# Optimization experiments

Hardware: AMD Instinct MI355X
Metric: run time of the kernel (lower is better)

Reference implementation:

```python
import jax, jax.numpy as jnp
import numpy as np

MIN_NORM = 1e-15
BALL_EPS = 4e-3  # float32 boundary eps used by the PoincareBall manifold


def _norm(x):
    return jnp.maximum(jnp.linalg.norm(x, axis=-1, keepdims=True), MIN_NORM)


def _artanh(x):
    # clamp like torch Artanh autograd fn (1e-7 margin)
    return jnp.arctanh(jnp.clip(x, -1.0 + 1e-7, 1.0 - 1e-7))


def proj(x, c):
    n = _norm(x)
    maxnorm = (1.0 - BALL_EPS) / jnp.sqrt(c)
    return jnp.where(n > maxnorm, x / n * maxnorm, x)


def expmap0(u, c):
    sc = jnp.sqrt(c)
    n = _norm(u)
    return jnp.tanh(sc * n) * u / (sc * n)


def logmap0(p, c):
    sc = jnp.sqrt(c)
    n = _norm(p)
    return _artanh(sc * n) * p / (sc * n)


def mobius_add(x, y, c):
    x2 = jnp.sum(x * x, axis=-1, keepdims=True)
    y2 = jnp.sum(y * y, axis=-1, keepdims=True)
    xy = jnp.sum(x * y, axis=-1, keepdims=True)
    num = (1.0 + 2.0 * c * xy + c * y2) * x + (1.0 - c * x2) * y
    denom = 1.0 + 2.0 * c * xy + c * c * x2 * y2
    return num / jnp.maximum(denom, MIN_NORM)


def mobius_matvec(m, x, c):
    sc = jnp.sqrt(c)
    xn = _norm(x)
    mx = x @ m.T  # [N, out]
    mxn = _norm(mx)
    res = jnp.tanh(mxn / xn * _artanh(sc * xn)) * mx / (mxn * sc)
    is_zero = jnp.all(mx == 0, axis=-1, keepdims=True)
    return jnp.where(is_zero, jnp.zeros_like(res), res)


def setup_inputs() -> dict:
    key = jax.random.key(0)
    N, D_IN, D_OUT, E = 100000, 128, 128, 1600000
    k1, k2, k3, k4, k5 = jax.random.split(key, 5)
    # points inside the Poincare ball (||x|| ~ 0.34 < 1)
    x = 0.03 * jax.random.normal(k1, (N, D_IN), dtype=jnp.float32)
    # xavier_uniform with gain sqrt(2)
    limit = np.sqrt(2.0) * np.sqrt(6.0 / (D_IN + D_OUT))
    weight = jax.random.uniform(k2, (D_OUT, D_IN), minval=-limit, maxval=limit, dtype=jnp.float32)
    bias = jnp.zeros((D_OUT,), dtype=jnp.float32)
    edge_index = jax.random.randint(k3, (2, E), 0, N, dtype=jnp.int64)
    edge_weight = jax.random.uniform(k4, (E,), dtype=jnp.float32) / 16.0
    return {"x": x, "weight": weight, "bias": bias,
            "edge_index": edge_index, "edge_weight": edge_weight,
            "num_nodes": N}


def reference(x, weight, bias, edge_index, edge_weight, num_nodes):
    c_in = 1.0
    c_out = 1.0
    # --- OriginHypLinear (dropout=0 / eval) ---
    mv = proj(mobius_matvec(weight, x, c_in), c_in)
    hyp_bias = proj(expmap0(bias[None, :], c_in), c_in)  # proj_tan0 is identity
    h = proj(mobius_add(mv, hyp_bias, c_in), c_in)
    # --- OriginHypAgg: logmap0 -> spmm -> expmap0 ---
    xt = logmap0(h, c_in)
    dst, src = edge_index[0], edge_index[1]
    support = jax.ops.segment_sum(edge_weight[:, None] * xt[src], dst,
                                  num_segments=num_nodes)
    h = proj(expmap0(support, c_in), c_in)
    # --- OriginHypAct: relu in tangent space ---
    xt = jax.nn.relu(logmap0(h, c_in))  # proj_tan0 identity
    return proj(expmap0(xt, c_out), c_out)
```

## Files before the change

kernel.cpp:

```cpp
#include <hip/hip_runtime.h>
#include <math.h>

#define D 128
#define MAXNORM 0.996f
#define MINNORM 1e-15f
#define ATCLAMP (1.0f - 1e-7f)

#define CHUNK 2048
#define BSH   7
#define MAXNB 1024
#define SCAP  6144

typedef unsigned int   u32;
typedef unsigned short u16;

typedef __attribute__((ext_vector_type(8))) short bf16x8;
typedef __attribute__((ext_vector_type(4))) float f32x4;

__device__ __forceinline__ float wsum(float v) {
#pragma unroll
  for (int m = 32; m; m >>= 1) v += __shfl_xor(v, m);
  return v;
}
__device__ __forceinline__ float rsum16(float v) {
#pragma unroll
  for (int m = 1; m <= 8; m <<= 1) v += __shfl_xor(v, m);
  return v;
}

__device__ __forceinline__ float frcp(float x) { return __builtin_amdgcn_rcpf(x); }

__device__ __forceinline__ float fast_artanh(float x) {
  x = fminf(x, ATCLAMP);
  return 0.5f * __logf((1.0f + x) * frcp(1.0f - x));
}
__device__ __forceinline__ float fast_tanh(float z) {
  float t = __expf(-2.0f * z);
  return (1.0f - t) * frcp(1.0f + t);
}

__device__ __forceinline__ float bflo(u32 u) { return __uint_as_float(u << 16); }
__device__ __forceinline__ float bfhi(u32 u) { return __uint_as_float(u & 0xffff0000u); }
__device__ __forceinline__ u16 f2bf(float f) {
  u32 u = __float_as_uint(f);
  return (u16)((u + 0x7fffu + ((u >> 16) & 1u)) >> 16);
}
__device__ __forceinline__ float bf2f(u16 h) { return __uint_as_float(((u32)h) << 16); }

union U4B8 { uint4 u; bf16x8 b; };
__device__ __forceinline__ bf16x8 as_b8(uint4 v) { U4B8 c; c.u = v; return c.b; }

__device__ __forceinline__ bool detect_bf16(const u32* p) {
  float lo = fabsf(bflo(p[threadIdx.x & 63]));
  return (bool)__all(lo < 1.0f);
}
__device__ __forceinline__ bool detect_i64(const int* p) {
  return (bool)__all(p[2 * (threadIdx.x & 63) + 1] == 0);
}

template<bool BF>
__device__ __forceinline__ void k1_body(const void* xv, const void* Wv,
                                        const void* bv, u16* xt, int N,
                                        uint4* Wh, uint4* Wl) {
  const int tid  = threadIdx.x;
  const int lane = tid & 63;
  const int wid  = tid >> 6;
  const int qg   = lane >> 4;
  const int lc   = lane & 15;

  for (int slot = tid; slot < 2048; slot += 256) {
    const int l = slot & 63, frag = slot >> 6;
    const int t = frag >> 2, ks = frag & 3;
    const int j  = (l & 15) + 16 * t;
    const int k0 = 32 * ks + 8 * (l >> 4);
    if (BF) {
      Wh[slot] = ((const uint4*)Wv)[j * 16 + (k0 >> 3)];
    } else {
      const float* Wf = (const float*)Wv;
      float4 f0 = *(const float4*)(Wf + (size_t)j * D + k0);
      float4 f1 = *(const float4*)(Wf + (size_t)j * D + k0 + 4);
      float f[8] = {f0.x, f0.y, f0.z, f0.w, f1.x, f1.y, f1.z, f1.w};
      u32 hw[4], lw[4];
#pragma unroll
      for (int i = 0; i < 4; ++i) {
        u16 h0 = f2bf(f[2*i]),  h1 = f2bf(f[2*i+1]);
        u16 l0 = f2bf(f[2*i]   - bf2f(h0));
        u16 l1 = f2bf(f[2*i+1] - bf2f(h1));
        hw[i] = (u32)h0 | ((u32)h1 << 16);
        lw[i] = (u32)l0 | ((u32)l1 << 16);
      }
      Wh[slot] = make_uint4(hw[0], hw[1], hw[2], hw[3]);
      Wl[slot] = make_uint4(lw[0], lw[1], lw[2], lw[3]);
    }
  }

  float bfr[8];
  float nb2 = 0.f;
#pragma unroll
  for (int t = 0; t < 8; ++t) {
    float v = BF ? bf2f(((const u16*)bv)[lc + 16 * t])
                 : ((const float*)bv)[lc + 16 * t];
    bfr[t] = v; nb2 += v * v;
  }
  nb2 = rsum16(nb2);
  float y2;
  {
    float nb = fmaxf(sqrtf(nb2), MINNORM);
    float s  = fast_tanh(nb) * frcp(nb);
    float n1 = s * nb;
    if (n1 > MAXNORM) s *= MAXNORM * frcp(n1);
#pragma unroll
    for (int t = 0; t < 8; ++t) bfr[t] *= s;
    y2 = s * s * nb2;
  }
  const bool bias_zero = (y2 == 0.0f);

  __syncthreads();

  const int tile  = blockIdx.x * 4 + wid;
  const int rbase = tile * 16;
  if (rbase >= N) return;

  int rowA = rbase + lc; if (rowA >= N) rowA = N - 1;
  uint4 Ah[4], Al[4];
  float xn2 = 0.f;
  if (BF) {
    const uint4* xr = (const uint4*)((const u16*)xv + (size_t)rowA * D);
#pragma unroll
    for (int ks = 0; ks < 4; ++ks) {
      uint4 v = xr[4 * ks + qg];
      Ah[ks] = v;
      float a0 = bflo(v.x), a1 = bfhi(v.x), a2 = bflo(v.y), a3 = bfhi(v.y);
      float a4 = bflo(v.z), a5 = bfhi(v.z), a6 = bflo(v.w), a7 = bfhi(v.w);
      xn2 += a0*a0 + a1*a1 + a2*a2 + a3*a3 + a4*a4 + a5*a5 + a6*a6 + a7*a7;
    }
  } else {
    const float4* xr = (const float4*)((const float*)xv + (size_t)rowA * D);
#pragma unroll
    for (int ks = 0; ks < 4; ++ks) {
      float4 f0 = xr[8 * ks + 2 * qg], f1 = xr[8 * ks + 2 * qg + 1];
      float f[8] = {f0.x, f0.y, f0.z, f0.w, f1.x, f1.y, f1.z, f1.w};
      u32 hw[4], lw[4];
#pragma unroll
      for (int i = 0; i < 4; ++i) {
        u16 h0 = f2bf(f[2*i]),  h1 = f2bf(f[2*i+1]);
        u16 l0 = f2bf(f[2*i]   - bf2f(h0));
        u16 l1 = f2bf(f[2*i+1] - bf2f(h1));
        hw[i] = (u32)h0 | ((u32)h1 << 16);
        lw[i] = (u32)l0 | ((u32)l1 << 16);
        xn2 += f[2*i] * f[2*i] + f[2*i+1] * f[2*i+1];
      }
      Ah[ks] = make_uint4(hw[0], hw[1], hw[2], hw[3]);
      Al[ks] = make_uint4(lw[0], lw[1], lw[2], lw[3]);
    }
  }
  xn2 += __shfl_xor(xn2, 16);
  xn2 += __shfl_xor(xn2, 32);

  f32x4 acc[8];
  const f32x4 zero = {0.f, 0.f, 0.f, 0.f};
#pragma unroll
  for (int t = 0; t < 8; ++t) acc[t] = zero;
#pragma unroll
  for (int ks = 0; ks < 4; ++ks) {
    bf16x8 a = as_b8(Ah[ks]);
    bf16x8 al;
    if (!BF) al = as_b8(Al[ks]);
#pragma unroll
    for (int t = 0; t < 8; ++t) {
      const int idx = (t * 4 + ks) * 64 + lane;
      bf16x8 bh = as_b8(Wh[idx]);
      acc[t] = __builtin_amdgcn_mfma_f32_16x16x32_bf16(a, bh, acc[t], 0, 0, 0);
      if (!BF) {
        bf16x8 bl = as_b8(Wl[idx]);
        acc[t] = __builtin_amdgcn_mfma_f32_16x16x32_bf16(al, bh, acc[t], 0, 0, 0);
        acc[t] = __builtin_amdgcn_mfma_f32_16x16x32_bf16(a,  bl, acc[t], 0, 0, 0);
      }
    }
  }

#pragma unroll
  for (int q = 0; q < 4; ++q) {
    const int row_off = qg * 4 + q;
    const int row = rbase + row_off;
    float xnq = fmaxf(sqrtf(__shfl(xn2, row_off)), MINNORM);
    float s2 = 0.f;
#pragma unroll
    for (int t = 0; t < 8; ++t) { float v = acc[t][q]; s2 += v * v; }
    s2 = rsum16(s2);
    float mxn = fmaxf(sqrtf(s2), MINNORM);
    float r = fast_tanh(mxn * frcp(xnq) * fast_artanh(xnq)) * frcp(mxn);
    float pn = r * mxn;
    if (pn > MAXNORM) { r *= MAXNORM * frcp(pn); pn = MAXNORM; }
    float h[8];
    float hn;
    if (bias_zero) {
#pragma unroll
      for (int t = 0; t < 8; ++t) h[t] = r * acc[t][q];
      hn = pn;
    } else {
      float xy = 0.f;
#pragma unroll
      for (int t = 0; t < 8; ++t) { h[t] = r * acc[t][q]; xy += h[t] * bfr[t]; }
      xy = rsum16(xy);
      float x2 = pn * pn;
      float ca = 1.f + 2.f * xy + y2;
      float cb = 1.f - x2;
      float id = frcp(fmaxf(1.f + 2.f * xy + x2 * y2, MINNORM));
      float s3 = 0.f;
#pragma unroll
      for (int t = 0; t < 8; ++t) { h[t] = (ca * h[t] + cb * bfr[t]) * id; s3 += h[t] * h[t]; }
      hn = fmaxf(sqrtf(rsum16(s3)), MINNORM);
    }
    float ps = (hn > MAXNORM) ? (MAXNORM * frcp(hn)) : 1.f;
    float np = fmaxf(hn * ps, MINNORM);
    float tsc = fast_artanh(np) * frcp(np) * ps;
    if (row < N) {
      u16* xo = xt + (size_t)row * D + lc;
#pragma unroll
      for (int t = 0; t < 8; ++t) xo[16 * t] = f2bf(tsc * h[t]);
    }
  }
}

extern "C" __global__ __launch_bounds__(256)
void OriginHyperbolicGraphConvolution_38628935860614_kernel(
    const void* x, const void* W, const void* b, u16* xt, int N) {
  __shared__ uint4 Wh[2048];
  __shared__ uint4 Wl[2048];
  if (detect_bf16((const u32*)x)) k1_body<true >(x, W, b, xt, N, Wh, Wl);
  else                            k1_body<false>(x, W, b, xt, N, Wh, Wl);
}

extern "C" __global__ __launch_bounds__(256) void ksA(
    const int* ei, const void* ew, uint2* ebuck, u16* soffs, int E, int N, int nb) {
  __shared__ int   hist[MAXNB];
  __shared__ int   sArr[MAXNB + 1];
  __shared__ int   psum[256];
  __shared__ uint2 recs[CHUNK];
  const bool i64 = detect_i64(ei);
  const bool bf  = detect_bf16((const u32*)ew);
  const int tid   = threadIdx.x;
  const int cbase = blockIdx.x * CHUNK;

  for (int i = tid; i < MAXNB; i += 256) hist[i] = 0;
  __syncthreads();

  int bkt[8], rank[8]; u32 px[8], wb[8]; bool val[8];
#pragma unroll
  for (int r = 0; r < 8; ++r) {
    const int e = cbase + r * 256 + tid;
    val[r] = false;
    if (e < E) {
      int dst, src;
      if (i64) { dst = ei[2 * (size_t)e]; src = ei[2 * ((size_t)E + e)]; }
      else     { dst = ei[e];             src = ei[(size_t)E + e]; }
      if ((unsigned)dst < (unsigned)N && (unsigned)src < (unsigned)N) {
        val[r] = true;
        bkt[r] = dst >> BSH;
        px[r]  = (u32)src | ((u32)(dst & ((1 << BSH) - 1)) << 17);
        float w;
        if (bf) w = bf2f(((const u16*)ew)[e]); else w = ((const float*)ew)[e];
        wb[r] = __float_as_uint(w);
        rank[r] = atomicAdd(&hist[bkt[r]], 1);
      }
    }
  }
  __syncthreads();

  const int g0 = tid * 4;
  int loc[4], ts = 0;
#pragma unroll
  for (int i = 0; i < 4; ++i) { loc[i] = ts; ts += hist[g0 + i]; }
  psum[tid] = ts; __syncthreads();
#pragma unroll
  for (int off = 1; off < 256; off <<= 1) {
    int t = (tid >= off) ? psum[tid - off] : 0;
    __syncthreads();
    psum[tid] += t;
    __syncthreads();
  }
  const int excl = psum[tid] - ts;
#pragma unroll
  for (int i = 0; i < 4; ++i) sArr[g0 + i] = excl + loc[i];
  if (tid == 255) sArr[MAXNB] = psum[255];
  __syncthreads();

#pragma unroll
  for (int r = 0; r < 8; ++r) if (val[r])
    recs[sArr[bkt[r]] + rank[r]] = make_uint2(px[r], wb[r]);
  __syncthreads();

  const int vcnt = sArr[MAXNB];
  for (int i = tid; i < vcnt; i += 256) ebuck[(size_t)cbase + i] = recs[i];
  u16* so = soffs + (size_t)blockIdx.x * (nb + 1);
  for (int b = tid; b <= nb; b += 256) so[b] = (u16)sArr[b];
}

extern "C" __global__ __launch_bounds__(256) void ks2sum(
    const u16* soffs, int* btot, int nb, int nchunks) {
  __shared__ int red[256];
  const int b = blockIdx.x, tid = threadIdx.x;
  int s = 0;
  for (int c = tid; c < nchunks; c += 256) {
    const u16* so = soffs + (size_t)c * (nb + 1) + b;
    s += (int)so[1] - (int)so[0];
  }
  red[tid] = s; __syncthreads();
#pragma unroll
  for (int off = 128; off; off >>= 1) {
    if (tid < off) red[tid] += red[tid + off];
    __syncthreads();
  }
  if (tid == 0) btot[b] = red[0];
}

extern "C" __global__ __launch_bounds__(1024) void ks2scan(
    const int* btot, int* bbase, int nb) {
  __shared__ int sc[1024];
  const int t = threadIdx.x;
  int v = (t < nb) ? btot[t] : 0;
  sc[t] = v; __syncthreads();
#pragma unroll
  for (int off = 1; off < 1024; off <<= 1) {
    int u = (t >= off) ? sc[t - off] : 0;
    __syncthreads();
    sc[t] += u;
    __syncthreads();
  }
  if (t < nb) bbase[t] = sc[t] - v;
  if (t == 1023) bbase[nb] = sc[1023];
}

extern "C" __global__ __launch_bounds__(256) void ks3(
    const uint2* ebuck, const u16* soffs, const int* bbase,
    uint2* esrt, int* offs, int N, int nb, int nchunks) {
  __shared__ uint2 stage[SCAP];
  __shared__ int hist[128], sc[128], cur[128];
  __shared__ int lcur;
  const int tid = threadIdx.x;
  const int b = blockIdx.x;
  const int s0 = bbase[b], s1 = bbase[b + 1], sz = s1 - s0;
  if (tid < 128) hist[tid] = 0;
  if (tid == 0) lcur = 0;
  __syncthreads();

  const bool fit = (sz <= SCAP);
  if (fit) {
    for (int c = tid; c < nchunks; c += 256) {
      const u16* so = soffs + (size_t)c * (nb + 1) + b;
      const int a = so[0], e = so[1];
      if (e > a) {
        const int base = atomicAdd(&lcur, e - a);
        for (int j = a; j < e; ++j) {
          const uint2 r = ebuck[(size_t)c * CHUNK + j];
          stage[base + (j - a)] = r;
          atomicAdd(&hist[(r.x >> 17) & 127], 1);
        }
      }
    }
  } else {
    for (int c = tid; c < nchunks; c += 256) {
      const u16* so = soffs + (size_t)c * (nb + 1) + b;
      for (int j = so[0]; j < so[1]; ++j)
        atomicAdd(&hist[(ebuck[(size_t)c * CHUNK + j].x >> 17) & 127], 1);
    }
  }
  __syncthreads();

  int v = 0;
  if (tid < 128) { v = hist[tid]; sc[tid] = v; }
  __syncthreads();
#pragma unroll
  for (int off = 1; off < 128; off <<= 1) {
    int t = (tid < 128 && tid >= off) ? sc[tid - off] : 0;
    __syncthreads();
    if (tid < 128) sc[tid] += t;
    __syncthreads();
  }
  if (tid < 128) {
    const int st = sc[tid] - v;
    cur[tid] = st;
    const int node = (b << BSH) + tid;
    if (node < N) offs[node] = s0 + st;
  }
  if (tid == 0 && b == nb - 1) offs[N] = s1;
  __syncthreads();

  if (fit) {
    for (int i = tid; i < sz; i += 256) {
      const uint2 r = stage[i];
      const int d = atomicAdd(&cur[(r.x >> 17) & 127], 1);
      esrt[s0 + d] = make_uint2(r.x & 0x1FFFFu, r.y);
    }
  } else {
    for (int c = tid; c < nchunks; c += 256) {
      const u16* so = soffs + (size_t)c * (nb + 1) + b;
      for (int j = so[0]; j < so[1]; ++j) {
        const uint2 r = ebuck[(size_t)c * CHUNK + j];
        const int d = atomicAdd(&cur[(r.x >> 17) & 127], 1);
        esrt[s0 + d] = make_uint2(r.x & 0x1FFFFu, r.y);
      }
    }
  }
}

extern "C" __global__ __launch_bounds__(256) void kagg(
    const int* offs, const uint2* esrt, const u16* xt,
    void* out, const void* xdet, int N) {
  const bool bf = detect_bf16((const u32*)xdet);
  const int lane = threadIdx.x & 63;
  const int node = blockIdx.x * 4 + (threadIdx.x >> 6);
  if (node >= N) return;
  int s0 = __builtin_amdgcn_readfirstlane(offs[node]);
  int s1 = __builtin_amdgcn_readfirstlane(offs[node + 1]);
  const uint2* ep = esrt + s0;
  const int cnt = s1 - s0;
  const u32* xtw = (const u32*)xt;
  float a0 = 0.f, a1 = 0.f;
  int i = 0;
  for (; i + 8 <= cnt; i += 8) {
    uint2 e[8]; u32 u[8];
#pragma unroll
    for (int k = 0; k < 8; ++k) e[k] = ep[i + k];
#pragma unroll
    for (int k = 0; k < 8; ++k) u[k] = xtw[(e[k].x << 6) | lane];
#pragma unroll
    for (int k = 0; k < 8; ++k) {
      const float w = __uint_as_float(e[k].y);
      a0 += w * bflo(u[k]);
      a1 += w * bfhi(u[k]);
    }
  }
  for (; i + 4 <= cnt; i += 4) {
    uint2 e[4]; u32 u[4];
#pragma unroll
    for (int k = 0; k < 4; ++k) e[k] = ep[i + k];
#pragma unroll
    for (int k = 0; k < 4; ++k) u[k] = xtw[(e[k].x << 6) | lane];
#pragma unroll
    for (int k = 0; k < 4; ++k) {
      const float w = __uint_as_float(e[k].y);
      a0 += w * bflo(u[k]);
      a1 += w * bfhi(u[k]);
    }
  }
  for (; i < cnt; ++i) {
    const uint2 e = ep[i];
    const u32 u = xtw[(e.x << 6) | lane];
    const float w = __uint_as_float(e.y);
    a0 += w * bflo(u);
    a1 += w * bfhi(u);
  }
  float n = fmaxf(sqrtf(wsum(a0 * a0 + a1 * a1)), MINNORM);
  float tn = fast_tanh(n);
  float m = tn * frcp(n);
  if (tn > MAXNORM) { m *= MAXNORM * frcp(tn); tn = MAXNORM; }
  float nn = fmaxf(tn, MINNORM);
  m *= fast_artanh(nn) * frcp(nn);
  float tA = fmaxf(m * a0, 0.f), tB = fmaxf(m * a1, 0.f);
  float nr = fmaxf(sqrtf(wsum(tA * tA + tB * tB)), MINNORM);
  float t2 = fast_tanh(nr);
  float m2 = t2 * frcp(nr);
  if (t2 > MAXNORM) m2 *= MAXNORM * frcp(t2);
  float oA = m2 * tA, oB = m2 * tB;
  if (bf) {
    u32 o = ((u32)f2bf(oA)) | (((u32)f2bf(oB)) << 16);
    ((u32*)out)[(size_t)node * 64 + lane] = o;
  } else {
    ((float2*)out)[(size_t)node * 64 + lane] = make_float2(oA, oB);
  }
}

extern "C" void kernel_launch(void* const* d_in, const int* in_sizes, int n_in,
                              void* d_out, int out_size, void* d_ws, size_t ws_size,
                              hipStream_t stream) {
  const void* x    = d_in[0];
  const void* W    = d_in[1];
  const void* bias = d_in[2];
  const int*  ei   = (const int*)d_in[3];
  const void* ew   = d_in[4];
  const int N = in_sizes[0] / D;
  const int E = in_sizes[4];
  const int nchunks = (E + CHUNK - 1) / CHUNK;
  const int nb      = (N + (1 << BSH) - 1) >> BSH;

  char* ws = (char*)d_ws;
  size_t off = 0;
  auto carve = [&](size_t bytes) { char* p = ws + off; off = (off + bytes + 255) & ~(size_t)255; return p; };
  u16*   xt     = (u16*)  carve((size_t)N * D * sizeof(u16));
  uint2* ebuck  = (uint2*)carve((size_t)nchunks * CHUNK * sizeof(uint2));
  uint2* esrt   = (uint2*)carve((size_t)E * sizeof(uint2));
  u16*   soffs  = (u16*)  carve((size_t)nchunks * (nb + 1) * sizeof(u16));
  int*   btot   = (int*)  carve((size_t)nb * sizeof(int));
  int*   bbase  = (int*)  carve((size_t)(nb + 1) * sizeof(int));
  int*   offs   = (int*)  carve((size_t)(N + 1) * sizeof(int));

  OriginHyperbolicGraphConvolution_38628935860614_kernel<<<(N + 63) / 64, 256, 0, stream>>>(
      x, W, bias, xt, N);
  ksA   <<<nchunks, 256, 0, stream>>>(ei, ew, ebuck, soffs, E, N, nb);
  ks2sum<<<nb, 256, 0, stream>>>(soffs, btot, nb, nchunks);
  ks2scan<<<1, 1024, 0, stream>>>(btot, bbase, nb);
  ks3   <<<nb, 256, 0, stream>>>(ebuck, soffs, bbase, esrt, offs, N, nb, nchunks);
  kagg  <<<(N + 3) / 4, 256, 0, stream>>>(offs, esrt, xt, d_out, x, N);
}
```

Baseline: 271.4 us.

## Replace chunked bucket sort with atomic-cursor fixed-capacity buckets and overflow path

Restructures the edge sort: ksA now appends each chunk's per-bucket runs into fixed-capacity per-bucket slots using global atomic cursors, with an overflow list for buckets beyond capacity. This removes the ks2sum and ks2scan kernels and the per-chunk offset table, so ks3 sorts each bucket in place and emits (start,count) pairs per node. The linear kernel also becomes grid-stride with a capped grid, and the aggregation loop unrolls to 16 edges. The cost is a zeroing kernel, atomic contention on the cursors, and a slow overflow scan if buckets exceed capacity.

```diff
diff --git a/kernel.cpp b/kernel.cpp
--- a/kernel.cpp
+++ b/kernel.cpp
@@ -9,7 +9,11 @@
 #define CHUNK 2048
 #define BSH   7
 #define MAXNB 1024
-#define SCAP  6144
+#define CAP   4096
+#define SCAP2 5120
+#define OCAP  262144
+#define TCAP  (1 << 20)
+#define CURSTRIDE 16
 
 typedef unsigned int   u32;
 typedef unsigned short u16;
@@ -56,6 +60,11 @@
 }
 __device__ __forceinline__ bool detect_i64(const int* p) {
   return (bool)__all(p[2 * (threadIdx.x & 63) + 1] == 0);
+}
+
+extern "C" __global__ __launch_bounds__(256) void k0_zeroi(int* p, int n) {
+  int i = blockIdx.x * 256 + threadIdx.x;
+  if (i < n) p[i] = 0;
 }
 
 template<bool BF>
@@ -117,108 +126,109 @@
 
   __syncthreads();
 
-  const int tile  = blockIdx.x * 4 + wid;
-  const int rbase = tile * 16;
-  if (rbase >= N) return;
-
-  int rowA = rbase + lc; if (rowA >= N) rowA = N - 1;
-  uint4 Ah[4], Al[4];
-  float xn2 = 0.f;
-  if (BF) {
-    const uint4* xr = (const uint4*)((const u16*)xv + (size_t)rowA * D);
+  const int T = (N + 15) >> 4;
+  for (int tile = blockIdx.x * 4 + wid; tile < T; tile += gridDim.x * 4) {
+    const int rbase = tile * 16;
+
+    int rowA = rbase + lc; if (rowA >= N) rowA = N - 1;
+    uint4 Ah[4], Al[4];
+    float xn2 = 0.f;
+    if (BF) {
+      const uint4* xr = (const uint4*)((const u16*)xv + (size_t)rowA * D);
+#pragma unroll
+      for (int ks = 0; ks < 4; ++ks) {
+        uint4 v = xr[4 * ks + qg];
+        Ah[ks] = v;
+        float a0 = bflo(v.x), a1 = bfhi(v.x), a2 = bflo(v.y), a3 = bfhi(v.y);
+        float a4 = bflo(v.z), a5 = bfhi(v.z), a6 = bflo(v.w), a7 = bfhi(v.w);
+        xn2 += a0*a0 + a1*a1 + a2*a2 + a3*a3 + a4*a4 + a5*a5 + a6*a6 + a7*a7;
+      }
+    } else {
+      const float4* xr = (const float4*)((const float*)xv + (size_t)rowA * D);
+#pragma unroll
+      for (int ks = 0; ks < 4; ++ks) {
+        float4 f0 = xr[8 * ks + 2 * qg], f1 = xr[8 * ks + 2 * qg + 1];
+        float f[8] = {f0.x, f0.y, f0.z, f0.w, f1.x, f1.y, f1.z, f1.w};
+        u32 hw[4], lw[4];
+#pragma unroll
+        for (int i = 0; i < 4; ++i) {
+          u16 h0 = f2bf(f[2*i]),  h1 = f2bf(f[2*i+1]);
+          u16 l0 = f2bf(f[2*i]   - bf2f(h0));
+          u16 l1 = f2bf(f[2*i+1] - bf2f(h1));
+          hw[i] = (u32)h0 | ((u32)h1 << 16);
+          lw[i] = (u32)l0 | ((u32)l1 << 16);
+          xn2 += f[2*i] * f[2*i] + f[2*i+1] * f[2*i+1];
+        }
+        Ah[ks] = make_uint4(hw[0], hw[1], hw[2], hw[3]);
+        Al[ks] = make_uint4(lw[0], lw[1], lw[2], lw[3]);
+      }
+    }
+    xn2 += __shfl_xor(xn2, 16);
+    xn2 += __shfl_xor(xn2, 32);
+
+    f32x4 acc[8];
+    const f32x4 zero = {0.f, 0.f, 0.f, 0.f};
+#pragma unroll
+    for (int t = 0; t < 8; ++t) acc[t] = zero;
 #pragma unroll
     for (int ks = 0; ks < 4; ++ks) {
-      uint4 v = xr[4 * ks + qg];
-      Ah[ks] = v;
-      float a0 = bflo(v.x), a1 = bfhi(v.x), a2 = bflo(v.y), a3 = bfhi(v.y);
-      float a4 = bflo(v.z), a5 = bfhi(v.z), a6 = bflo(v.w), a7 = bfhi(v.w);
-      xn2 += a0*a0 + a1*a1 + a2*a2 + a3*a3 + a4*a4 + a5*a5 + a6*a6 + a7*a7;
-    }
-  } else {
-    const float4* xr = (const float4*)((const float*)xv + (size_t)rowA * D);
-#pragma unroll
-    for (int ks = 0; ks < 4; ++ks) {
-      float4 f0 = xr[8 * ks + 2 * qg], f1 = xr[8 * ks + 2 * qg + 1];
-      float f[8] = {f0.x, f0.y, f0.z, f0.w, f1.x, f1.y, f1.z, f1.w};
-      u32 hw[4], lw[4];
-#pragma unroll
-      for (int i = 0; i < 4; ++i) {
-        u16 h0 = f2bf(f[2*i]),  h1 = f2bf(f[2*i+1]);
-        u16 l0 = f2bf(f[2*i]   - bf2f(h0));
-        u16 l1 = f2bf(f[2*i+1] - bf2f(h1));
-        hw[i] = (u32)h0 | ((u32)h1 << 16);
-        lw[i] = (u32)l0 | ((u32)l1 << 16);
-        xn2 += f[2*i] * f[2*i] + f[2*i+1] * f[2*i+1];
-      }
-      Ah[ks] = make_uint4(hw[0], hw[1], hw[2], hw[3]);
-      Al[ks] = make_uint4(lw[0], lw[1], lw[2], lw[3]);
-    }
-  }
-  xn2 += __shfl_xor(xn2, 16);
-  xn2 += __shfl_xor(xn2, 32);
-
-  f32x4 acc[8];
-  const f32x4 zero = {0.f, 0.f, 0.f, 0.f};
-#pragma unroll
-  for (int t = 0; t < 8; ++t) acc[t] = zero;
-#pragma unroll
-  for (int ks = 0; ks < 4; ++ks) {
-    bf16x8 a = as_b8(Ah[ks]);
-    bf16x8 al;
-    if (!BF) al = as_b8(Al[ks]);
-#pragma unroll
-    for (int t = 0; t < 8; ++t) {
-      const int idx = (t * 4 + ks) * 64 + lane;
-      bf16x8 bh = as_b8(Wh[idx]);
-      acc[t] = __builtin_amdgcn_mfma_f32_16x16x32_bf16(a, bh, acc[t], 0, 0, 0);
-      if (!BF) {
-        bf16x8 bl = as_b8(Wl[idx]);
-        acc[t] = __builtin_amdgcn_mfma_f32_16x16x32_bf16(al, bh, acc[t], 0, 0, 0);
-        acc[t] = __builtin_amdgcn_mfma_f32_16x16x32_bf16(a,  bl, acc[t], 0, 0, 0);
-      }
-    }
-  }
-
-#pragma unroll
-  for (int q = 0; q < 4; ++q) {
-    const int row_off = qg * 4 + q;
-    const int row = rbase + row_off;
-    float xnq = fmaxf(sqrtf(__shfl(xn2, row_off)), MINNORM);
-    float s2 = 0.f;
-#pragma unroll
-    for (int t = 0; t < 8; ++t) { float v = acc[t][q]; s2 += v * v; }
-    s2 = rsum16(s2);
-    float mxn = fmaxf(sqrtf(s2), MINNORM);
-    float r = fast_tanh(mxn * frcp(xnq) * fast_artanh(xnq)) * frcp(mxn);
-    float pn = r * mxn;
-    if (pn > MAXNORM) { r *= MAXNORM * frcp(pn); pn = MAXNORM; }
-    float h[8];
-    float hn;
-    if (bias_zero) {
-#pragma unroll
-      for (int t = 0; t < 8; ++t) h[t] = r * acc[t][q];
-      hn = pn;
-    } else {
-      float xy = 0.f;
-#pragma unroll
-      for (int t = 0; t < 8; ++t) { h[t] = r * acc[t][q]; xy += h[t] * bfr[t]; }
-      xy = rsum16(xy);
-      float x2 = pn * pn;
-      float ca = 1.f + 2.f * xy + y2;
-      float cb = 1.f - x2;
-      float id = frcp(fmaxf(1.f + 2.f * xy + x2 * y2, MINNORM));
-      float s3 = 0.f;
-#pragma unroll
-      for (int t = 0; t < 8; ++t) { h[t] = (ca * h[t] + cb * bfr[t]) * id; s3 += h[t] * h[t]; }
-      hn = fmaxf(sqrtf(rsum16(s3)), MINNORM);
-    }
-    float ps = (hn > MAXNORM) ? (MAXNORM * frcp(hn)) : 1.f;
-    float np = fmaxf(hn * ps, MINNORM);
-    float tsc = fast_artanh(np) * frcp(np) * ps;
-    if (row < N) {
-      u16* xo = xt + (size_t)row * D + lc;
-#pragma unroll
-      for (int t = 0; t < 8; ++t) xo[16 * t] = f2bf(tsc * h[t]);
+      bf16x8 a = as_b8(Ah[ks]);
+      bf16x8 al;
+      if (!BF) al = as_b8(Al[ks]);
+#pragma unroll
+      for (int t = 0; t < 8; ++t) {
+        const int idx = (t * 4 + ks) * 64 + lane;
+        bf16x8 bh = as_b8(Wh[idx]);
+        acc[t] = __builtin_amdgcn_mfma_f32_16x16x32_bf16(a, bh, acc[t], 0, 0, 0);
+        if (!BF) {
+          bf16x8 bl = as_b8(Wl[idx]);
+          acc[t] = __builtin_amdgcn_mfma_f32_16x16x32_bf16(al, bh, acc[t], 0, 0, 0);
+          acc[t] = __builtin_amdgcn_mfma_f32_16x16x32_bf16(a,  bl, acc[t], 0, 0, 0);
+        }
+      }
+    }
+
+#pragma unroll
+    for (int q = 0; q < 4; ++q) {
+      const int row_off = qg * 4 + q;
+      const int row = rbase + row_off;
+      float xnq = fmaxf(sqrtf(__shfl(xn2, row_off)), MINNORM);
+      float s2 = 0.f;
+#pragma unroll
+      for (int t = 0; t < 8; ++t) { float v = acc[t][q]; s2 += v * v; }
+      s2 = rsum16(s2);
+      float mxn = fmaxf(sqrtf(s2), MINNORM);
+      float r = fast_tanh(mxn * frcp(xnq) * fast_artanh(xnq)) * frcp(mxn);
+      float pn = r * mxn;
+      if (pn > MAXNORM) { r *= MAXNORM * frcp(pn); pn = MAXNORM; }
+      float h[8];
+      float hn;
+      if (bias_zero) {
+#pragma unroll
+        for (int t = 0; t < 8; ++t) h[t] = r * acc[t][q];
+        hn = pn;
+      } else {
+        float xy = 0.f;
+#pragma unroll
+        for (int t = 0; t < 8; ++t) { h[t] = r * acc[t][q]; xy += h[t] * bfr[t]; }
+        xy = rsum16(xy);
+        float x2 = pn * pn;
+        float ca = 1.f + 2.f * xy + y2;
+        float cb = 1.f - x2;
+        float id = frcp(fmaxf(1.f + 2.f * xy + x2 * y2, MINNORM));
+        float s3 = 0.f;
+#pragma unroll
+        for (int t = 0; t < 8; ++t) { h[t] = (ca * h[t] + cb * bfr[t]) * id; s3 += h[t] * h[t]; }
+        hn = fmaxf(sqrtf(rsum16(s3)), MINNORM);
+      }
+      float ps = (hn > MAXNORM) ? (MAXNORM * frcp(hn)) : 1.f;
+      float np = fmaxf(hn * ps, MINNORM);
+      float tsc = fast_artanh(np) * frcp(np) * ps;
+      if (row < N) {
+        u16* xo = xt + (size_t)row * D + lc;
+#pragma unroll
+        for (int t = 0; t < 8; ++t) xo[16 * t] = f2bf(tsc * h[t]);
+      }
     }
   }
 }
@@ -233,7 +243,8 @@
 }
 
 extern "C" __global__ __launch_bounds__(256) void ksA(
-    const int* ei, const void* ew, uint2* ebuck, u16* soffs, int E, int N, int nb) {
+    const int* ei, const void* ew, uint2* ebuck, int* cursor,
+    uint2* ofl, int* oflb, int* oflcnt, int E, int N, int nb) {
   __shared__ int   hist[MAXNB];
   __shared__ int   sArr[MAXNB + 1];
   __shared__ int   psum[256];
@@ -253,8 +264,12 @@
     val[r] = false;
     if (e < E) {
       int dst, src;
-      if (i64) { dst = ei[2 * (size_t)e]; src = ei[2 * ((size_t)E + e)]; }
-      else     { dst = ei[e];             src = ei[(size_t)E + e]; }
+      if (i64) {
+        dst = (int)((const uint2*)ei)[(size_t)e].x;
+        src = (int)((const uint2*)ei)[(size_t)E + e].x;
+      } else {
+        dst = ei[e]; src = ei[(size_t)E + e];
+      }
       if ((unsigned)dst < (unsigned)N && (unsigned)src < (unsigned)N) {
         val[r] = true;
         bkt[r] = dst >> BSH;
@@ -291,80 +306,59 @@
     recs[sArr[bkt[r]] + rank[r]] = make_uint2(px[r], wb[r]);
   __syncthreads();
 
-  const int vcnt = sArr[MAXNB];
-  for (int i = tid; i < vcnt; i += 256) ebuck[(size_t)cbase + i] = recs[i];
-  u16* so = soffs + (size_t)blockIdx.x * (nb + 1);
-  for (int b = tid; b <= nb; b += 256) so[b] = (u16)sArr[b];
-}
-
-extern "C" __global__ __launch_bounds__(256) void ks2sum(
-    const u16* soffs, int* btot, int nb, int nchunks) {
-  __shared__ int red[256];
-  const int b = blockIdx.x, tid = threadIdx.x;
-  int s = 0;
-  for (int c = tid; c < nchunks; c += 256) {
-    const u16* so = soffs + (size_t)c * (nb + 1) + b;
-    s += (int)so[1] - (int)so[0];
-  }
-  red[tid] = s; __syncthreads();
-#pragma unroll
-  for (int off = 128; off; off >>= 1) {
-    if (tid < off) red[tid] += red[tid + off];
-    __syncthreads();
-  }
-  if (tid == 0) btot[b] = red[0];
-}
-
-extern "C" __global__ __launch_bounds__(1024) void ks2scan(
-    const int* btot, int* bbase, int nb) {
-  __shared__ int sc[1024];
-  const int t = threadIdx.x;
-  int v = (t < nb) ? btot[t] : 0;
-  sc[t] = v; __syncthreads();
-#pragma unroll
-  for (int off = 1; off < 1024; off <<= 1) {
-    int u = (t >= off) ? sc[t - off] : 0;
-    __syncthreads();
-    sc[t] += u;
-    __syncthreads();
-  }
-  if (t < nb) bbase[t] = sc[t] - v;
-  if (t == 1023) bbase[nb] = sc[1023];
+  for (int b = tid; b < nb; b += 256) {
+    const int a = sArr[b], len = sArr[b + 1] - a;
+    if (len == 0) continue;
+    const int pos = atomicAdd(&cursor[b * CURSTRIDE], len);
+    for (int j = 0; j < len; ++j) {
+      const uint2 r = recs[a + j];
+      const int p = pos + j;
+      if (p < CAP) ebuck[(size_t)b * CAP + p] = r;
+      else {
+        const int op = atomicAdd(oflcnt, 1);
+        if (op < OCAP) { ofl[op] = r; oflb[op] = b; }
+      }
+    }
+  }
 }
 
 extern "C" __global__ __launch_bounds__(256) void ks3(
-    const uint2* ebuck, const u16* soffs, const int* bbase,
-    uint2* esrt, int* offs, int N, int nb, int nchunks) {
-  __shared__ uint2 stage[SCAP];
+    uint2* ebuck, const int* cursor, const uint2* ofl, const int* oflb,
+    const int* oflcnt, int* tailcur, uint2* offs2, int N, int nb) {
+  __shared__ uint2 stage[SCAP2];
   __shared__ int hist[128], sc[128], cur[128];
-  __shared__ int lcur;
+  __shared__ int extr, tb;
   const int tid = threadIdx.x;
   const int b = blockIdx.x;
-  const int s0 = bbase[b], s1 = bbase[b + 1], sz = s1 - s0;
+  const int cnt = cursor[b * CURSTRIDE];
+  const int inslot = min(cnt, CAP);
+  uint2* seg = ebuck + (size_t)b * CAP;
+  const int nof = min(*oflcnt, OCAP);
+  const int node0 = b << BSH;
   if (tid < 128) hist[tid] = 0;
-  if (tid == 0) lcur = 0;
-  __syncthreads();
-
-  const bool fit = (sz <= SCAP);
+  if (tid == 0) extr = inslot;
+  __syncthreads();
+
+  const bool fit = (cnt <= SCAP2);
   if (fit) {
-    for (int c = tid; c < nchunks; c += 256) {
-      const u16* so = soffs + (size_t)c * (nb + 1) + b;
-      const int a = so[0], e = so[1];
-      if (e > a) {
-        const int base = atomicAdd(&lcur, e - a);
-        for (int j = a; j < e; ++j) {
-          const uint2 r = ebuck[(size_t)c * CHUNK + j];
-          stage[base + (j - a)] = r;
-          atomicAdd(&hist[(r.x >> 17) & 127], 1);
-        }
+    for (int i = tid; i < inslot; i += 256) {
+      const uint2 r = seg[i];
+      stage[i] = r;
+      atomicAdd(&hist[(r.x >> 17) & 127], 1);
+    }
+    if (cnt > CAP) {
+      for (int i = tid; i < nof; i += 256) if (oflb[i] == b) {
+        const int p = atomicAdd(&extr, 1);
+        const uint2 r = ofl[i];
+        stage[p] = r;
+        atomicAdd(&hist[(r.x >> 17) & 127], 1);
       }
     }
   } else {
-    for (int c = tid; c < nchunks; c += 256) {
-      const u16* so = soffs + (size_t)c * (nb + 1) + b;
-      for (int j = so[0]; j < so[1]; ++j)
-        atomicAdd(&hist[(ebuck[(size_t)c * CHUNK + j].x >> 17) & 127], 1);
-    }
+    for (int i = tid; i < inslot; i += 256)
+      atomicAdd(&hist[(seg[i].x >> 17) & 127], 1);
+    for (int i = tid; i < nof; i += 256) if (oflb[i] == b)
+      atomicAdd(&hist[(ofl[i].x >> 17) & 127], 1);
   }
   __syncthreads();
 
@@ -378,55 +372,60 @@
     if (tid < 128) sc[tid] += t;
     __syncthreads();
   }
+  if (tid == 0) tb = (cnt <= CAP) ? -1 : atomicAdd(tailcur, cnt);
+  __syncthreads();
+  const size_t base = (tb < 0) ? (size_t)b * CAP : ((size_t)nb * CAP + (size_t)tb);
   if (tid < 128) {
     const int st = sc[tid] - v;
     cur[tid] = st;
-    const int node = (b << BSH) + tid;
-    if (node < N) offs[node] = s0 + st;
-  }
-  if (tid == 0 && b == nb - 1) offs[N] = s1;
+    const int node = node0 + tid;
+    if (node < N) offs2[node] = make_uint2((u32)(base + st), (u32)v);
+  }
   __syncthreads();
 
   if (fit) {
-    for (int i = tid; i < sz; i += 256) {
+    const int tot = extr;
+    for (int i = tid; i < tot; i += 256) {
       const uint2 r = stage[i];
       const int d = atomicAdd(&cur[(r.x >> 17) & 127], 1);
-      esrt[s0 + d] = make_uint2(r.x & 0x1FFFFu, r.y);
+      ebuck[base + d] = make_uint2(r.x & 0x1FFFFu, r.y);
     }
   } else {
-    for (int c = tid; c < nchunks; c += 256) {
-      const u16* so = soffs + (size_t)c * (nb + 1) + b;
-      for (int j = so[0]; j < so[1]; ++j) {
-        const uint2 r = ebuck[(size_t)c * CHUNK + j];
-        const int d = atomicAdd(&cur[(r.x >> 17) & 127], 1);
-        esrt[s0 + d] = make_uint2(r.x & 0x1FFFFu, r.y);
-      }
+    for (int i = tid; i < inslot; i += 256) {
+      const uint2 r = seg[i];
+      const int d = atomicAdd(&cur[(r.x >> 17) & 127], 1);
+      ebuck[base + d] = make_uint2(r.x & 0x1FFFFu, r.y);
+    }
+    for (int i = tid; i < nof; i += 256) if (oflb[i] == b) {
+      const uint2 r = ofl[i];
+      const int d = atomicAdd(&cur[(r.x >> 17) & 127], 1);
+      ebuck[base + d] = make_uint2(r.x & 0x1FFFFu, r.y);
     }
   }
 }
 
 extern "C" __global__ __launch_bounds__(256) void kagg(
-    const int* offs, const uint2* esrt, const u16* xt,
+    const uint2* offs2, const uint2* ebuck, const u16* xt,
     void* out, const void* xdet, int N) {
   const bool bf = detect_bf16((const u32*)xdet);
   const int lane = threadIdx.x & 63;
   const int node = blockIdx.x * 4 + (threadIdx.x >> 6);
   if (node >= N) return;
-  int s0 = __builtin_amdgcn_readfirstlane(offs[node]);
-  int s1 = __builtin_amdgcn_readfirstlane(offs[node + 1]);
-  const uint2* ep = esrt + s0;
-  const int cnt = s1 - s0;
+  const uint2 oo = offs2[node];
+  const int s0  = __builtin_amdgcn_readfirstlane((int)oo.x);
+  const int cnt = __builtin_amdgcn_readfirstlane((int)oo.y);
+  const uint2* ep = ebuck + s0;
   const u32* xtw = (const u32*)xt;
   float a0 = 0.f, a1 = 0.f;
   int i = 0;
-  for (; i + 8 <= cnt; i += 8) {
-    uint2 e[8]; u32 u[8];
-#pragma unroll
-    for (int k = 0; k < 8; ++k) e[k] = ep[i + k];
-#pragma unroll
-    for (int k = 0; k < 8; ++k) u[k] = xtw[(e[k].x << 6) | lane];
-#pragma unroll
-    for (int k = 0; k < 8; ++k) {
+  for (; i + 16 <= cnt; i += 16) {
+    uint2 e[16]; u32 u[16];
+#pragma unroll
+    for (int k = 0; k < 16; ++k) e[k] = ep[i + k];
+#pragma unroll
+    for (int k = 0; k < 16; ++k) u[k] = xtw[(e[k].x << 6) | lane];
+#pragma unroll
+    for (int k = 0; k < 16; ++k) {
       const float w = __uint_as_float(e[k].y);
       a0 += w * bflo(u[k]);
       a1 += w * bfhi(u[k]);
@@ -488,19 +487,24 @@
   char* ws = (char*)d_ws;
   size_t off = 0;
   auto carve = [&](size_t bytes) { char* p = ws + off; off = (off + bytes + 255) & ~(size_t)255; return p; };
-  u16*   xt     = (u16*)  carve((size_t)N * D * sizeof(u16));
-  uint2* ebuck  = (uint2*)carve((size_t)nchunks * CHUNK * sizeof(uint2));
-  uint2* esrt   = (uint2*)carve((size_t)E * sizeof(uint2));
-  u16*   soffs  = (u16*)  carve((size_t)nchunks * (nb + 1) * sizeof(u16));
-  int*   btot   = (int*)  carve((size_t)nb * sizeof(int));
-  int*   bbase  = (int*)  carve((size_t)(nb + 1) * sizeof(int));
-  int*   offs   = (int*)  carve((size_t)(N + 1) * sizeof(int));
-
-  OriginHyperbolicGraphConvolution_38628935860614_kernel<<<(N + 63) / 64, 256, 0, stream>>>(
+  u16*   xt    = (u16*)  carve((size_t)N * D * sizeof(u16));
+  uint2* ebuck = (uint2*)carve(((size_t)nb * CAP + TCAP) * sizeof(uint2));
+  uint2* ofl   = (uint2*)carve((size_t)OCAP * sizeof(uint2));
+  int*   oflb  = (int*)  carve((size_t)OCAP * sizeof(int));
+  uint2* offs2 = (uint2*)carve((size_t)N * sizeof(uint2));
+  int*   czone = (int*)  carve(((size_t)nb * CURSTRIDE + 2) * sizeof(int));
+  int*   cursor  = czone;
+  int*   oflcnt  = czone + (size_t)nb * CURSTRIDE;
+  int*   tailcur = oflcnt + 1;
+
+  const int nz = nb * CURSTRIDE + 2;
+  const int T  = (N + 15) / 16;
+  const int g1 = min((T + 3) / 4, 512);
+
+  k0_zeroi<<<(nz + 255) / 256, 256, 0, stream>>>(czone, nz);
+  OriginHyperbolicGraphConvolution_38628935860614_kernel<<<g1, 256, 0, stream>>>(
       x, W, bias, xt, N);
-  ksA   <<<nchunks, 256, 0, stream>>>(ei, ew, ebuck, soffs, E, N, nb);
-  ks2sum<<<nb, 256, 0, stream>>>(soffs, btot, nb, nchunks);
-  ks2scan<<<1, 1024, 0, stream>>>(btot, bbase, nb);
-  ks3   <<<nb, 256, 0, stream>>>(ebuck, soffs, bbase, esrt, offs, N, nb, nchunks);
-  kagg  <<<(N + 3) / 4, 256, 0, stream>>>(offs, esrt, xt, d_out, x, N);
-}
+  ksA <<<nchunks, 256, 0, stream>>>(ei, ew, ebuck, cursor, ofl, oflb, oflcnt, E, N, nb);
+  ks3 <<<nb, 256, 0, stream>>>(ebuck, cursor, ofl, oflb, oflcnt, tailcur, offs2, N, nb);
+  kagg<<<(N + 3) / 4, 256, 0, stream>>>(offs2, ebuck, xt, d_out, x, N);
+}
```

Result: slower. 291.0 us (+7.2%).
